# Performance work log

Hardware: AMD Instinct MI355X
Metric: run time of the kernel (lower is better)

## Reference

```python
import jax, jax.numpy as jnp
import numpy as np

D_IN = 1024
D_OUT = 1024
N_HEADS = 16
HEAD_DIM = D_OUT // N_HEADS


def setup_inputs() -> dict:
    key = jax.random.key(0)
    ks = jax.random.split(key, 6)
    s = 0.02
    x = jax.random.normal(ks[0], (2, 2048, D_IN), dtype=jnp.float32)
    Wq = jax.random.normal(ks[1], (D_IN, D_OUT), dtype=jnp.float32) * s
    Wk = jax.random.normal(ks[2], (D_IN, D_OUT), dtype=jnp.float32) * s
    Wv = jax.random.normal(ks[3], (D_IN, D_OUT), dtype=jnp.float32) * s
    Wo = jax.random.normal(ks[4], (D_OUT, D_OUT), dtype=jnp.float32) * s
    bo = jax.random.normal(ks[5], (D_OUT,), dtype=jnp.float32) * s
    return {"x": x, "Wq": Wq, "Wk": Wk, "Wv": Wv, "Wo": Wo, "bo": bo}


def reference(x, Wq, Wk, Wv, Wo, bo):
    B, S, _ = x.shape
    # project and split heads: (B, H, S, Dh)
    def split(t):
        return t.reshape(B, S, N_HEADS, HEAD_DIM).transpose(0, 2, 1, 3)
    q = split(x @ Wq)
    k = split(x @ Wk)
    v = split(x @ Wv)
    scores = jnp.einsum('bhqd,bhkd->bhqk', q, k)  # (B,H,S,S)
    causal = jnp.tril(jnp.ones((S, S), dtype=bool))
    scores = jnp.where(causal, scores, -jnp.inf)
    attn = jax.nn.softmax(scores / np.sqrt(HEAD_DIM).astype(np.float32), axis=-1)
    ctx = jnp.einsum('bhqk,bhkd->bhqd', attn, v)
    ctx = ctx.transpose(0, 2, 1, 3).reshape(B, S, D_OUT)
    return ctx @ Wo + bo
```

## Files before the change

kernel.cpp:

```cpp
#include <hip/hip_runtime.h>
#include <hip/hip_bf16.h>
#include <math.h>

typedef __attribute__((ext_vector_type(8))) short bf16x8;
typedef __attribute__((ext_vector_type(8))) unsigned short u16x8;
typedef __attribute__((ext_vector_type(4))) float f32x4;

__device__ __forceinline__ unsigned short f2bf(float f) {
  union { float f; unsigned u; } c; c.f = f;
  unsigned u = c.u;
  u += 0x7fffu + ((u >> 16) & 1u);
  return (unsigned short)(u >> 16);
}
__device__ __forceinline__ unsigned fb(float x) {
  union { float f; unsigned u; } c; c.f = x; return c.u;
}
__device__ __forceinline__ void async16(const unsigned short* g, unsigned short* l) {
  __builtin_amdgcn_global_load_lds(
      (const __attribute__((address_space(1))) unsigned int*)g,
      (__attribute__((address_space(3))) unsigned int*)l, 16, 0, 0);
}

__global__ __launch_bounds__(256) void cast_kernel(const float* __restrict__ in,
                                                   unsigned short* __restrict__ out,
                                                   int n4) {
  int i = blockIdx.x * 256 + threadIdx.x;
  if (i >= n4) return;
  float4 v = ((const float4*)in)[i];
  ushort4 o;
  o.x = f2bf(v.x); o.y = f2bf(v.y); o.z = f2bf(v.z); o.w = f2bf(v.w);
  ((ushort4*)out)[i] = o;
}

__global__ __launch_bounds__(256) void transpose_cast(
    const float* __restrict__ Wq, const float* __restrict__ Wk,
    const float* __restrict__ Wv, const float* __restrict__ Wo,
    unsigned short* __restrict__ Wqkvt, unsigned short* __restrict__ Wot) {
  __shared__ float t[32][33];
  int z = blockIdx.z;
  const float* src = (z == 0) ? Wq : (z == 1) ? Wk : (z == 2) ? Wv : Wo;
  unsigned short* dst = (z < 3) ? (Wqkvt + (size_t)z * 1024 * 1024) : Wot;
  int tx = threadIdx.x & 31, ty = threadIdx.x >> 5;
  int bx = blockIdx.x, by = blockIdx.y;
#pragma unroll
  for (int i = 0; i < 4; ++i)
    t[ty + i * 8][tx] = src[(size_t)(by * 32 + ty + i * 8) * 1024 + bx * 32 + tx];
  __syncthreads();
#pragma unroll
  for (int i = 0; i < 4; ++i)
    dst[(size_t)(bx * 32 + ty + i * 8) * 1024 + by * 32 + tx] = f2bf(t[tx][ty + i * 8]);
}

__global__ __launch_bounds__(256) void gemm_qkv(
    const unsigned short* __restrict__ A, const unsigned short* __restrict__ Bt,
    unsigned short* __restrict__ Qh, unsigned short* __restrict__ Kh,
    unsigned short* __restrict__ Vt, int K) {
  __shared__ unsigned short As [128][32];
  __shared__ unsigned short As2[128][32];
  __shared__ unsigned short Bs [128][32];
  __shared__ unsigned short Bs2[128][32];
  const int flat = blockIdx.x;
  const int xcd = flat & 7, idx = flat >> 3;
  const int mg = xcd >> 1, ng = xcd & 1;
  const int m0 = (mg * 8 + (idx & 7)) * 128;
  const int n0 = (ng * 12 + (idx >> 3)) * 128;
  const int tid = threadIdx.x;
  const int wave = tid >> 6, lane = tid & 63;
  const int quad = lane >> 4, l16 = lane & 15;
  const int wm = (wave >> 1) * 64, wn = (wave & 1) * 64;
  const int srow = tid >> 2, sch = (tid & 3) * 8;
  f32x4 acc[4][4] = {};

  for (int k0 = 0; k0 < K; k0 += 64) {
    __syncthreads();
    async16(A  + (size_t)(m0 + srow) * K + k0 + sch,           &As [srow][sch]);
    async16(A  + (size_t)(m0 + srow + 64) * K + k0 + sch,      &As [srow + 64][sch]);
    async16(A  + (size_t)(m0 + srow) * K + k0 + 32 + sch,      &As2[srow][sch]);
    async16(A  + (size_t)(m0 + srow + 64) * K + k0 + 32 + sch, &As2[srow + 64][sch]);
    async16(Bt + (size_t)(n0 + srow) * K + k0 + sch,           &Bs [srow][sch]);
    async16(Bt + (size_t)(n0 + srow + 64) * K + k0 + sch,      &Bs [srow + 64][sch]);
    async16(Bt + (size_t)(n0 + srow) * K + k0 + 32 + sch,      &Bs2[srow][sch]);
    async16(Bt + (size_t)(n0 + srow + 64) * K + k0 + 32 + sch, &Bs2[srow + 64][sch]);
    __syncthreads();
    bf16x8 af[4], bfr[4];
#pragma unroll
    for (int i = 0; i < 4; ++i) {
      af[i]  = *(const bf16x8*)&As[wm + i * 16 + l16][quad * 8];
      bfr[i] = *(const bf16x8*)&Bs[wn + i * 16 + l16][quad * 8];
    }
#pragma unroll
    for (int mi = 0; mi < 4; ++mi)
#pragma unroll
      for (int ni = 0; ni < 4; ++ni)
        acc[mi][ni] = __builtin_amdgcn_mfma_f32_16x16x32_bf16(af[mi], bfr[ni], acc[mi][ni], 0, 0, 0);
#pragma unroll
    for (int i = 0; i < 4; ++i) {
      af[i]  = *(const bf16x8*)&As2[wm + i * 16 + l16][quad * 8];
      bfr[i] = *(const bf16x8*)&Bs2[wn + i * 16 + l16][quad * 8];
    }
#pragma unroll
    for (int mi = 0; mi < 4; ++mi)
#pragma unroll
      for (int ni = 0; ni < 4; ++ni)
        acc[mi][ni] = __builtin_amdgcn_mfma_f32_16x16x32_bf16(af[mi], bfr[ni], acc[mi][ni], 0, 0, 0);
  }

#pragma unroll
  for (int mi = 0; mi < 4; ++mi) {
#pragma unroll
    for (int ni = 0; ni < 4; ++ni) {
      const int col = n0 + wn + ni * 16 + l16;
      const int token0 = m0 + wm + mi * 16 + quad * 4;
      const int bb = token0 >> 11, s0 = token0 & 2047;
      if (col < 2048) {
        const int hh = (col & 1023) >> 6, d = col & 63;
        unsigned short* dst = (col < 1024) ? Qh : Kh;
        dst += ((size_t)(bb * 16 + hh) * 2048 + s0) * 64 + d;
#pragma unroll
        for (int r = 0; r < 4; ++r) dst[(size_t)r * 64] = f2bf(acc[mi][ni][r]);
      } else {
        const int vc = col - 2048, hh = vc >> 6, d = vc & 63;
        ushort4 us;
        us.x = f2bf(acc[mi][ni][0]); us.y = f2bf(acc[mi][ni][1]);
        us.z = f2bf(acc[mi][ni][2]); us.w = f2bf(acc[mi][ni][3]);
        *(ushort4*)&Vt[(((size_t)(bb * 16 + hh) * 64 + (s0 >> 5)) * 64 + d) * 32 + (s0 & 31)] = us;
      }
    }
  }
}

__global__ __launch_bounds__(256) void gemm_out(
    const unsigned short* __restrict__ A, const unsigned short* __restrict__ Bt,
    float* __restrict__ C, const float* __restrict__ bias, int N, int K) {
  __shared__ unsigned short As [128][32];
  __shared__ unsigned short As2[128][32];
  __shared__ unsigned short Bs [64][32];
  __shared__ unsigned short Bs2[64][32];
  const int flat = blockIdx.x;
  const int xcd = flat & 7, idx = flat >> 3;
  const int mg = xcd >> 1, ng = xcd & 1;
  const int m0 = (mg * 8 + (idx & 7)) * 128;
  const int n0 = (ng * 8 + (idx >> 3)) * 64;
  const int tid = threadIdx.x;
  const int wave = tid >> 6, lane = tid & 63;
  const int quad = lane >> 4, l16 = lane & 15;
  const int wm = (wave >> 1) * 64, wn = (wave & 1) * 32;
  const int srow = tid >> 2, sch = (tid & 3) * 8;
  f32x4 acc[4][2] = {};

  for (int k0 = 0; k0 < K; k0 += 64) {
    __syncthreads();
    async16(A  + (size_t)(m0 + srow) * K + k0 + sch,           &As [srow][sch]);
    async16(A  + (size_t)(m0 + srow + 64) * K + k0 + sch,      &As [srow + 64][sch]);
    async16(A  + (size_t)(m0 + srow) * K + k0 + 32 + sch,      &As2[srow][sch]);
    async16(A  + (size_t)(m0 + srow + 64) * K + k0 + 32 + sch, &As2[srow + 64][sch]);
    async16(Bt + (size_t)(n0 + srow) * K + k0 + sch,           &Bs [srow][sch]);
    async16(Bt + (size_t)(n0 + srow) * K + k0 + 32 + sch,      &Bs2[srow][sch]);
    __syncthreads();
    bf16x8 af[4], bfr[2];
#pragma unroll
    for (int i = 0; i < 4; ++i)
      af[i] = *(const bf16x8*)&As[wm + i * 16 + l16][quad * 8];
#pragma unroll
    for (int i = 0; i < 2; ++i)
      bfr[i] = *(const bf16x8*)&Bs[wn + i * 16 + l16][quad * 8];
#pragma unroll
    for (int mi = 0; mi < 4; ++mi)
#pragma unroll
      for (int ni = 0; ni < 2; ++ni)
        acc[mi][ni] = __builtin_amdgcn_mfma_f32_16x16x32_bf16(af[mi], bfr[ni], acc[mi][ni], 0, 0, 0);
#pragma unroll
    for (int i = 0; i < 4; ++i)
      af[i] = *(const bf16x8*)&As2[wm + i * 16 + l16][quad * 8];
#pragma unroll
    for (int i = 0; i < 2; ++i)
      bfr[i] = *(const bf16x8*)&Bs2[wn + i * 16 + l16][quad * 8];
#pragma unroll
    for (int mi = 0; mi < 4; ++mi)
#pragma unroll
      for (int ni = 0; ni < 2; ++ni)
        acc[mi][ni] = __builtin_amdgcn_mfma_f32_16x16x32_bf16(af[mi], bfr[ni], acc[mi][ni], 0, 0, 0);
  }
#pragma unroll
  for (int mi = 0; mi < 4; ++mi)
#pragma unroll
    for (int ni = 0; ni < 2; ++ni) {
      const int col = n0 + wn + ni * 16 + l16;
      const float bv = bias[col];
      const int row0 = m0 + wm + mi * 16 + quad * 4;
#pragma unroll
      for (int r = 0; r < 4; ++r)
        C[(size_t)(row0 + r) * N + col] = acc[mi][ni][r] + bv;
    }
}

__global__ __launch_bounds__(128, 3) void attn_kernel(
    const unsigned short* __restrict__ Qh, const unsigned short* __restrict__ Kh,
    const unsigned short* __restrict__ Vt, unsigned short* __restrict__ ctx) {
  const int id = blockIdx.x;
  const int j = id >> 3;
  const int bh = (id & 7) | ((j & 3) << 3);
  const int s = 63 - (j >> 2);
  const int b = bh >> 4, h = bh & 15;
  const int wave = threadIdx.x >> 6, lane = threadIdx.x & 63;
  const int quad = lane >> 4, l16 = lane & 15;
  const int q0 = s * 32;
  const int T = (s + 2) >> 1;
  const int lo = wave ? (T >> 1) : 0;
  const int hi = wave ? T : (T >> 1);

  __shared__ __align__(16) char smem[10752];
  unsigned short (*Pt)[32][72] = (unsigned short (*)[32][72])smem;
  float (*Os)[2][64][4] = (float (*)[2][64][4])smem;
  float (*Ms)[64] = (float (*)[64])(smem + 10240);

  const unsigned short* Qp = Qh + (size_t)bh * 2048 * 64;
  const unsigned short* Kg = Kh + (size_t)bh * 2048 * 64;
  const unsigned short* Vg = Vt + (size_t)bh * 64 * 2048;

  bf16x8 qf[2][2];
#pragma unroll
  for (int qg = 0; qg < 2; ++qg)
#pragma unroll
    for (int kk = 0; kk < 2; ++kk)
      qf[qg][kk] = *(const bf16x8*)(Qp + (size_t)(q0 + qg * 16 + l16) * 64 + kk * 32 + quad * 8);

  bf16x8 ones;
#pragma unroll
  for (int jj = 0; jj < 8; ++jj) ones[jj] = (short)0x3F80;

  f32x4 o[5][2] = {};
  float m_[2] = {-INFINITY, -INFINITY};
  const float C = 0.18033688f;

  for (int jt = lo; jt < hi; ++jt) {
    const int k0 = jt * 64;
    f32x4 st[4][2] = {};
#pragma unroll
    for (int keyg = 0; keyg < 4; ++keyg) {
#pragma unroll
      for (int kk = 0; kk < 2; ++kk) {
        bf16x8 kf = *(const bf16x8*)(Kg + (size_t)(k0 + keyg * 16 + l16) * 64 + kk * 32 + quad * 8);
#pragma unroll
        for (int qg = 0; qg < 2; ++qg)
          st[keyg][qg] = __builtin_amdgcn_mfma_f32_16x16x32_bf16(kf, qf[qg][kk], st[keyg][qg], 0, 0, 0);
      }
    }
    bf16x8 vf[4][2];
#pragma unroll
    for (int dg = 0; dg < 4; ++dg)
#pragma unroll
      for (int half = 0; half < 2; ++half)
        vf[dg][half] = *(const bf16x8*)(Vg + (size_t)(2 * jt + half) * 2048 + (dg * 16 + l16) * 32 + quad * 8);
    if (jt == T - 1) {
#pragma unroll
      for (int keyg = 0; keyg < 4; ++keyg)
#pragma unroll
        for (int r = 0; r < 4; ++r) {
          const int key = k0 + keyg * 16 + quad * 4 + r;
#pragma unroll
          for (int qg = 0; qg < 2; ++qg)
            if (key > q0 + qg * 16 + l16) st[keyg][qg][r] = -INFINITY;
        }
    }
    float al[2];
#pragma unroll
    for (int qg = 0; qg < 2; ++qg) {
      float mx = fmaxf(fmaxf(st[0][qg][0], st[0][qg][1]), fmaxf(st[0][qg][2], st[0][qg][3]));
#pragma unroll
      for (int keyg = 1; keyg < 4; ++keyg)
        mx = fmaxf(mx, fmaxf(fmaxf(st[keyg][qg][0], st[keyg][qg][1]),
                             fmaxf(st[keyg][qg][2], st[keyg][qg][3])));
      mx = fmaxf(mx, __shfl_xor(mx, 16));
      mx = fmaxf(mx, __shfl_xor(mx, 32));
      const float mn = fmaxf(m_[qg], mx * C);
      al[qg] = exp2f(m_[qg] - mn);
      m_[qg] = mn;
#pragma unroll
      for (int keyg = 0; keyg < 4; ++keyg) {
        float p0 = exp2f(fmaf(st[keyg][qg][0], C, -mn));
        float p1 = exp2f(fmaf(st[keyg][qg][1], C, -mn));
        float p2 = exp2f(fmaf(st[keyg][qg][2], C, -mn));
        float p3 = exp2f(fmaf(st[keyg][qg][3], C, -mn));
        uint2 pk;
        pk.x = __builtin_amdgcn_perm(fb(p1), fb(p0), 0x07060302u);
        pk.y = __builtin_amdgcn_perm(fb(p3), fb(p2), 0x07060302u);
        *(uint2*)&Pt[wave][qg * 16 + l16][keyg * 16 + quad * 4] = pk;
      }
    }
    if (__any(fminf(al[0], al[1]) < 1.0f)) {
#pragma unroll
      for (int dg = 0; dg < 5; ++dg)
#pragma unroll
        for (int qg = 0; qg < 2; ++qg)
#pragma unroll
          for (int r = 0; r < 4; ++r) o[dg][qg][r] *= al[qg];
    }
    bf16x8 pb[2][2];
#pragma unroll
    for (int qg = 0; qg < 2; ++qg)
#pragma unroll
      for (int half = 0; half < 2; ++half)
        pb[qg][half] = *(const bf16x8*)&Pt[wave][qg * 16 + l16][half * 32 + quad * 8];
#pragma unroll
    for (int dg = 0; dg < 4; ++dg)
#pragma unroll
      for (int qg = 0; qg < 2; ++qg) {
        o[dg][qg] = __builtin_amdgcn_mfma_f32_16x16x32_bf16(vf[dg][0], pb[qg][0], o[dg][qg], 0, 0, 0);
        o[dg][qg] = __builtin_amdgcn_mfma_f32_16x16x32_bf16(vf[dg][1], pb[qg][1], o[dg][qg], 0, 0, 0);
      }
#pragma unroll
    for (int qg = 0; qg < 2; ++qg) {
      o[4][qg] = __builtin_amdgcn_mfma_f32_16x16x32_bf16(ones, pb[qg][0], o[4][qg], 0, 0, 0);
      o[4][qg] = __builtin_amdgcn_mfma_f32_16x16x32_bf16(ones, pb[qg][1], o[4][qg], 0, 0, 0);
    }
  }
  __syncthreads();
  if (wave == 1) {
#pragma unroll
    for (int qg = 0; qg < 2; ++qg) {
      Ms[qg][lane] = m_[qg];
#pragma unroll
      for (int dg = 0; dg < 5; ++dg)
        *(f32x4*)&Os[dg][qg][lane][0] = o[dg][qg];
    }
  }
  __syncthreads();
  if (wave == 0) {
#pragma unroll
    for (int qg = 0; qg < 2; ++qg) {
      const float m1 = Ms[qg][lane];
      const float mn = fmaxf(m_[qg], m1);
      const float a0 = exp2f(m_[qg] - mn), a1 = exp2f(m1 - mn);
#pragma unroll
      for (int dg = 0; dg < 5; ++dg) {
        f32x4 o1 = *(const f32x4*)&Os[dg][qg][lane][0];
#pragma unroll
        for (int r = 0; r < 4; ++r) o[dg][qg][r] = o[dg][qg][r] * a0 + o1[r] * a1;
      }
      const float inv = 1.f / o[4][qg][0];
      const size_t base = (size_t)(b * 2048 + q0 + qg * 16 + l16) * 1024 + h * 64;
#pragma unroll
      for (int dg = 0; dg < 4; ++dg) {
        ushort4 us;
        us.x = f2bf(o[dg][qg][0] * inv); us.y = f2bf(o[dg][qg][1] * inv);
        us.z = f2bf(o[dg][qg][2] * inv); us.w = f2bf(o[dg][qg][3] * inv);
        *(ushort4*)&ctx[base + dg * 16 + quad * 4] = us;
      }
    }
  }
}

extern "C" void kernel_launch(void* const* d_in, const int* in_sizes, int n_in,
                              void* d_out, int out_size, void* d_ws, size_t ws_size,
                              hipStream_t stream) {
  const float* x  = (const float*)d_in[0];
  const float* Wq = (const float*)d_in[1];
  const float* Wk = (const float*)d_in[2];
  const float* Wv = (const float*)d_in[3];
  const float* Wo = (const float*)d_in[4];
  const float* bo = (const float*)d_in[5];
  float* out = (float*)d_out;

  char* ws = (char*)d_ws;
  unsigned short* Xb    = (unsigned short*)(ws);
  unsigned short* Wqkvt = (unsigned short*)(ws + (size_t)8  * 1048576);
  unsigned short* Wot   = (unsigned short*)(ws + (size_t)14 * 1048576);
  unsigned short* Qhb   = (unsigned short*)(ws + (size_t)16 * 1048576);
  unsigned short* Khb   = (unsigned short*)(ws + (size_t)24 * 1048576);
  unsigned short* Vtb   = (unsigned short*)(ws + (size_t)32 * 1048576);
  unsigned short* CT    = (unsigned short*)(ws + (size_t)40 * 1048576);

  cast_kernel<<<4096, 256, 0, stream>>>(x, Xb, 1048576);
  transpose_cast<<<dim3(32, 32, 4), 256, 0, stream>>>(Wq, Wk, Wv, Wo, Wqkvt, Wot);
  gemm_qkv<<<768, 256, 0, stream>>>(Xb, Wqkvt, Qhb, Khb, Vtb, 1024);
  attn_kernel<<<2048, 128, 0, stream>>>(Qhb, Khb, Vtb, CT);
  gemm_out<<<512, 256, 0, stream>>>(CT, Wot, out, bo, 1024, 1024);
}
```

Baseline: 191.0 us.

## Split attention KV range across four waves with tree reduction of partials

The attention block grows from two to four waves. Each wave processes a quarter of the causal KV tiles for the 32-query block, and the four partial softmax states are merged through shared memory in a two-level tree reduction. This is meant to shorten the serial KV loop per block and add latency hiding. In exchange it doubles shared memory, adds extra barriers and merge work, and may lower occupancy under the new launch bounds. The merge also skips exp2 when a partial already holds the max.

```diff
diff --git a/kernel.cpp b/kernel.cpp
--- a/kernel.cpp
+++ b/kernel.cpp
@@ -194,7 +194,7 @@
     }
 }
 
-__global__ __launch_bounds__(128, 3) void attn_kernel(
+__global__ __launch_bounds__(256, 3) void attn_kernel(
     const unsigned short* __restrict__ Qh, const unsigned short* __restrict__ Kh,
     const unsigned short* __restrict__ Vt, unsigned short* __restrict__ ctx) {
   const int id = blockIdx.x;
@@ -206,13 +206,11 @@
   const int quad = lane >> 4, l16 = lane & 15;
   const int q0 = s * 32;
   const int T = (s + 2) >> 1;
-  const int lo = wave ? (T >> 1) : 0;
-  const int hi = wave ? T : (T >> 1);
-
-  __shared__ __align__(16) char smem[10752];
+  const int lo = (T * wave) >> 2;
+  const int hi = (T * (wave + 1)) >> 2;
+
+  __shared__ __align__(16) char smem[21504];
   unsigned short (*Pt)[32][72] = (unsigned short (*)[32][72])smem;
-  float (*Os)[2][64][4] = (float (*)[2][64][4])smem;
-  float (*Ms)[64] = (float (*)[64])(smem + 10240);
 
   const unsigned short* Qp = Qh + (size_t)bh * 2048 * 64;
   const unsigned short* Kg = Kh + (size_t)bh * 2048 * 64;
@@ -315,8 +313,16 @@
       o[4][qg] = __builtin_amdgcn_mfma_f32_16x16x32_bf16(ones, pb[qg][1], o[4][qg], 0, 0, 0);
     }
   }
+
+  float (*Os0)[2][64][4] = (float (*)[2][64][4])(smem);
+  float (*Ms0)[64]       = (float (*)[64])(smem + 10240);
+  float (*Os1)[2][64][4] = (float (*)[2][64][4])(smem + 10752);
+  float (*Ms1)[64]       = (float (*)[64])(smem + 10752 + 10240);
+
   __syncthreads();
-  if (wave == 1) {
+  if (wave == 1 || wave == 3) {
+    float (*Os)[2][64][4] = (wave == 1) ? Os0 : Os1;
+    float (*Ms)[64]       = (wave == 1) ? Ms0 : Ms1;
 #pragma unroll
     for (int qg = 0; qg < 2; ++qg) {
       Ms[qg][lane] = m_[qg];
@@ -326,15 +332,45 @@
     }
   }
   __syncthreads();
-  if (wave == 0) {
+  if (wave == 0 || wave == 2) {
+    float (*Os)[2][64][4] = (wave == 0) ? Os0 : Os1;
+    float (*Ms)[64]       = (wave == 0) ? Ms0 : Ms1;
 #pragma unroll
     for (int qg = 0; qg < 2; ++qg) {
       const float m1 = Ms[qg][lane];
       const float mn = fmaxf(m_[qg], m1);
-      const float a0 = exp2f(m_[qg] - mn), a1 = exp2f(m1 - mn);
+      const float a0 = (m_[qg] == mn) ? 1.f : exp2f(m_[qg] - mn);
+      const float a1 = (m1 == mn) ? 1.f : exp2f(m1 - mn);
 #pragma unroll
       for (int dg = 0; dg < 5; ++dg) {
         f32x4 o1 = *(const f32x4*)&Os[dg][qg][lane][0];
+#pragma unroll
+        for (int r = 0; r < 4; ++r) o[dg][qg][r] = o[dg][qg][r] * a0 + o1[r] * a1;
+      }
+      m_[qg] = mn;
+    }
+  }
+  __syncthreads();
+  if (wave == 2) {
+#pragma unroll
+    for (int qg = 0; qg < 2; ++qg) {
+      Ms0[qg][lane] = m_[qg];
+#pragma unroll
+      for (int dg = 0; dg < 5; ++dg)
+        *(f32x4*)&Os0[dg][qg][lane][0] = o[dg][qg];
+    }
+  }
+  __syncthreads();
+  if (wave == 0) {
+#pragma unroll
+    for (int qg = 0; qg < 2; ++qg) {
+      const float m1 = Ms0[qg][lane];
+      const float mn = fmaxf(m_[qg], m1);
+      const float a0 = (m_[qg] == mn) ? 1.f : exp2f(m_[qg] - mn);
+      const float a1 = (m1 == mn) ? 1.f : exp2f(m1 - mn);
+#pragma unroll
+      for (int dg = 0; dg < 5; ++dg) {
+        f32x4 o1 = *(const f32x4*)&Os0[dg][qg][lane][0];
 #pragma unroll
         for (int r = 0; r < 4; ++r) o[dg][qg][r] = o[dg][qg][r] * a0 + o1[r] * a1;
       }
@@ -374,6 +410,6 @@
   cast_kernel<<<4096, 256, 0, stream>>>(x, Xb, 1048576);
   transpose_cast<<<dim3(32, 32, 4), 256, 0, stream>>>(Wq, Wk, Wv, Wo, Wqkvt, Wot);
   gemm_qkv<<<768, 256, 0, stream>>>(Xb, Wqkvt, Qhb, Khb, Vtb, 1024);
-  attn_kernel<<<2048, 128, 0, stream>>>(Qhb, Khb, Vtb, CT);
+  attn_kernel<<<2048, 256, 0, stream>>>(Qhb, Khb, Vtb, CT);
   gemm_out<<<512, 256, 0, stream>>>(CT, Wot, out, bo, 1024, 1024);
 }
```

Result: no change. 191.3 us (+0.2%).
